# Optimization experiments

Hardware: AMD Instinct MI355X
Metric: run time of the kernel (lower is better)

Reference implementation:

```python
import jax, jax.numpy as jnp
import numpy as np


def setup_inputs() -> dict:
    key = jax.random.key(0)
    k_x, k_q, k_k, k_v = jax.random.split(key, 4)
    B, S, E, D = 4, 2048, 1024, 1024
    scale = 1.0 / np.sqrt(E)
    return {
        "x": jax.random.normal(k_x, (B, S, E), dtype=jnp.float32),
        # nn.Linear weight matrices, shape [out_dim, in_dim]; y = x @ W.T
        "w_q": jax.random.normal(k_q, (D, E), dtype=jnp.float32) * scale,
        "w_k": jax.random.normal(k_k, (D, E), dtype=jnp.float32) * scale,
        "w_v": jax.random.normal(k_v, (D, E), dtype=jnp.float32) * scale,
    }


def reference(x, w_q, w_k, w_v):
    # x: [B, S, E]; w_*: [D, E] (torch nn.Linear convention)
    B, S, E = x.shape
    q = jnp.einsum("bse,de->bsd", x, w_q)  # [B, S, D]
    k = jnp.einsum("bse,de->bsd", x, w_k)
    v = jnp.einsum("bse,de->bsd", x, w_v)
    D = q.shape[-1]
    # raw scores, then causal mask (strictly upper triangle -> -inf), then
    # scale by 1/sqrt(D) inside softmax exactly as the original does.
    scores = jnp.einsum("bsd,btd->bst", q, k)  # [B, S, S]
    causal = jnp.tril(jnp.ones((S, S), dtype=bool))  # True = keep
    scores = jnp.where(causal[None], scores, -jnp.inf)
    attn = jax.nn.softmax(scores / jnp.sqrt(jnp.asarray(D, x.dtype)), axis=-1)
    # dropout p=0.0 -> identity
    return jnp.einsum("bst,btd->bsd", attn, v)  # [B, S, D]
```

## Files before the change

kernel.cpp:

```cpp
#include <hip/hip_runtime.h>
#include <hip/hip_bf16.h>


typedef unsigned short u16;
typedef __attribute__((ext_vector_type(4))) u16   u16x4;
typedef __attribute__((ext_vector_type(8))) u16   u16x8;
typedef __attribute__((ext_vector_type(8))) short short8;
typedef __attribute__((ext_vector_type(4))) float f32x4;

__device__ inline u16 f2b(float v) {
    __hip_bfloat16 b = __float2bfloat16(v);
    return *reinterpret_cast<u16*>(&b);
}
__device__ inline float b2f(u16 v) {
    unsigned int u = ((unsigned int)v) << 16;
    return *reinterpret_cast<float*>(&u);
}

template <typename T> __device__ inline void store_elem(T* p, float v);
template <> __device__ inline void store_elem<float>(float* p, float v) { *p = v; }
template <> __device__ inline void store_elem<u16>(u16* p, float v)     { *p = f2b(v); }

__device__ inline void gload_lds16(const u16* g, u16* l) {
    __builtin_amdgcn_global_load_lds(
        (const __attribute__((address_space(1))) void*)g,
        (__attribute__((address_space(3))) void*)l, 16, 0, 0);
}

__device__ __forceinline__ short8 dsr128(const u16* p) {
    short8 d;
    asm volatile("ds_read_b128 %0, %1"
        : "=v"(d)
        : "v"((unsigned)(unsigned long long)
              (const __attribute__((address_space(3))) u16*)p));
    return d;
}

__global__ __launch_bounds__(256) void cast_all_kernel(
    const float* __restrict__ x,  const float* __restrict__ wq,
    const float* __restrict__ wk, const float* __restrict__ wv,
    u16* __restrict__ dst) {
    int q = blockIdx.x * 256 + threadIdx.x;
    const float* src;
    int sidx;
    if (q < 2097152) { src = x; sidx = q * 4; }
    else {
        int qq = q - 2097152;
        int w  = qq >> 18;
        sidx   = (qq & 262143) * 4;
        src    = (w == 0) ? wq : (w == 1) ? wk : wv;
    }
    float4 v = *(const float4*)(src + sidx);
    u16x4 o;
    o.x = f2b(v.x); o.y = f2b(v.y); o.z = f2b(v.z); o.w = f2b(v.w);
    *(u16x4*)(dst + q * 4) = o;
}

__device__ __forceinline__ void gemm256_core(
    u16* __restrict__ lds,
    const u16* __restrict__ Ab, int lda,
    const u16* __restrict__ Bb, int ldb,
    u16* __restrict__ Cb, int ldc,
    int m0, int n0)
{
    const int tid  = threadIdx.x;
    const int lane = tid & 63;
    const int wave = tid >> 6;
    const int quad = lane >> 4;
    const int r16  = lane & 15;
    const int wm   = wave >> 2;
    const int wn   = wave & 3;

    int gA[2][2], gB[2][2], lA[2][2], lB[2][2];
    {
        const int cswz = ((lane & 3) * 8) ^ (((lane >> 5) & 1) << 4);
        const int rsub = lane >> 2;
#pragma unroll
        for (int u = 0; u < 2; ++u)
#pragma unroll
            for (int j = 0; j < 2; ++j) {
                int s   = j * 8 + wave;
                int sh  = s >> 1, cg = s & 1;
                int rgA = (sh & 3) + (sh >> 2) * 8 + u * 4;
                int rgB = sh + u * 8;
                int cl  = cg * 32 + cswz;
                gA[u][j] = (m0 + rgA * 16 + rsub) * lda + cl;
                gB[u][j] = (n0 + rgB * 16 + rsub) * ldb + cl;
                lA[u][j] = (rgA * 2 + cg) * 512 + lane * 8;
                lB[u][j] = (rgB * 2 + cg) * 512 + lane * 8;
            }
    }

#define STAGE_A(BUF, U, KK) do { \
        gload_lds16(Ab + gA[U][0] + (KK), lds + (BUF)*32768 + lA[U][0]); \
        gload_lds16(Ab + gA[U][1] + (KK), lds + (BUF)*32768 + lA[U][1]); } while (0)
#define STAGE_B(BUF, U, KK) do { \
        gload_lds16(Bb + gB[U][0] + (KK), lds + (BUF)*32768 + 16384 + lB[U][0]); \
        gload_lds16(Bb + gB[U][1] + (KK), lds + (BUF)*32768 + 16384 + lB[U][1]); } while (0)

    const int cswr = (quad * 8) ^ ((r16 >> 3) << 4);
    const int rdA0 = wm * 16 * 512 + r16 * 32 + cswr;
    const int rdB0 = wn * 8  * 512 + r16 * 32 + cswr;

    f32x4 acc[8][4] = {};

    STAGE_B(0, 0, 0);  STAGE_B(0, 1, 0);  STAGE_A(0, 0, 0);  STAGE_A(0, 1, 0);
    STAGE_B(1, 0, 64); STAGE_B(1, 1, 64); STAGE_A(1, 0, 64); STAGE_A(1, 1, 64);
    asm volatile("s_waitcnt vmcnt(8)" ::: "memory");
    __builtin_amdgcn_s_barrier();

    for (int t = 0; t < 16; ++t) {
        const int  buf = t & 1;
        const int  kk2 = t * 64 + 128;
        const bool pf  = (t < 14);
        const u16* Al  = lds + buf * 32768;
        const u16* Bl  = lds + buf * 32768 + 16384;
        short8 bfr[4][2], a01[2][2], a23[2][2], a45[2][2], a67[2][2];

#pragma unroll
        for (int nf = 0; nf < 4; ++nf)
#pragma unroll
            for (int ks = 0; ks < 2; ++ks)
                bfr[nf][ks] = dsr128(&Bl[rdB0 + (nf * 2 + ks) * 512]);
#pragma unroll
        for (int mf = 0; mf < 2; ++mf)
#pragma unroll
            for (int ks = 0; ks < 2; ++ks)
                a01[mf][ks] = dsr128(&Al[rdA0 + (mf * 2 + ks) * 512]);
        __builtin_amdgcn_s_barrier();
#pragma unroll
        for (int mf = 0; mf < 2; ++mf)
#pragma unroll
            for (int ks = 0; ks < 2; ++ks)
                a23[mf][ks] = dsr128(&Al[rdA0 + ((mf + 2) * 2 + ks) * 512]);
        asm volatile("s_waitcnt lgkmcnt(4)" ::: "memory");
        __builtin_amdgcn_sched_barrier(0);
        __builtin_amdgcn_s_setprio(1);
#pragma unroll
        for (int mf = 0; mf < 2; ++mf)
#pragma unroll
            for (int nf = 0; nf < 4; ++nf)
#pragma unroll
                for (int ks = 0; ks < 2; ++ks)
                    acc[mf][nf] = __builtin_amdgcn_mfma_f32_16x16x32_bf16(
                        a01[mf][ks], bfr[nf][ks], acc[mf][nf], 0, 0, 0);
        __builtin_amdgcn_s_setprio(0);
        __builtin_amdgcn_s_barrier();

        if (pf) STAGE_B(buf, 0, kk2);
        __builtin_amdgcn_s_barrier();
#pragma unroll
        for (int mf = 0; mf < 2; ++mf)
#pragma unroll
            for (int ks = 0; ks < 2; ++ks)
                a45[mf][ks] = dsr128(&Al[rdA0 + ((mf + 4) * 2 + ks) * 512]);
        asm volatile("s_waitcnt lgkmcnt(4)" ::: "memory");
        __builtin_amdgcn_sched_barrier(0);
        __builtin_amdgcn_s_setprio(1);
#pragma unroll
        for (int mf = 0; mf < 2; ++mf)
#pragma unroll
            for (int nf = 0; nf < 4; ++nf)
#pragma unroll
                for (int ks = 0; ks < 2; ++ks)
                    acc[mf + 2][nf] = __builtin_amdgcn_mfma_f32_16x16x32_bf16(
                        a23[mf][ks], bfr[nf][ks], acc[mf + 2][nf], 0, 0, 0);
        __builtin_amdgcn_s_setprio(0);
        __builtin_amdgcn_s_barrier();

        if (pf) { STAGE_B(buf, 1, kk2); STAGE_A(buf, 0, kk2); }
        __builtin_amdgcn_s_barrier();
#pragma unroll
        for (int mf = 0; mf < 2; ++mf)
#pragma unroll
            for (int ks = 0; ks < 2; ++ks)
                a67[mf][ks] = dsr128(&Al[rdA0 + ((mf + 6) * 2 + ks) * 512]);
        asm volatile("s_waitcnt lgkmcnt(4)" ::: "memory");
        __builtin_amdgcn_sched_barrier(0);
        __builtin_amdgcn_s_setprio(1);
#pragma unroll
        for (int mf = 0; mf < 2; ++mf)
#pragma unroll
            for (int nf = 0; nf < 4; ++nf)
#pragma unroll
                for (int ks = 0; ks < 2; ++ks)
                    acc[mf + 4][nf] = __builtin_amdgcn_mfma_f32_16x16x32_bf16(
                        a45[mf][ks], bfr[nf][ks], acc[mf + 4][nf], 0, 0, 0);
        __builtin_amdgcn_s_setprio(0);
        __builtin_amdgcn_s_barrier();

        __builtin_amdgcn_s_barrier();
        asm volatile("s_waitcnt lgkmcnt(0)" ::: "memory");
        __builtin_amdgcn_sched_barrier(0);
        __builtin_amdgcn_s_setprio(1);
#pragma unroll
        for (int mf = 0; mf < 2; ++mf)
#pragma unroll
            for (int nf = 0; nf < 4; ++nf)
#pragma unroll
                for (int ks = 0; ks < 2; ++ks)
                    acc[mf + 6][nf] = __builtin_amdgcn_mfma_f32_16x16x32_bf16(
                        a67[mf][ks], bfr[nf][ks], acc[mf + 6][nf], 0, 0, 0);
        __builtin_amdgcn_s_setprio(0);
        if (pf) STAGE_A(buf, 1, kk2);
        if (pf) asm volatile("s_waitcnt vmcnt(8)" ::: "memory");
        else    asm volatile("s_waitcnt vmcnt(0)" ::: "memory");
        __builtin_amdgcn_s_barrier();
    }
#undef STAGE_A
#undef STAGE_B

#pragma unroll
    for (int mf = 0; mf < 8; ++mf) {
        int m = m0 + wm * 128 + mf * 16 + quad * 4;
#pragma unroll
        for (int nf = 0; nf < 4; ++nf) {
            int n = n0 + wn * 64 + nf * 16 + r16;
#pragma unroll
            for (int r = 0; r < 4; ++r)
                Cb[(m + r) * ldc + n] = f2b(acc[mf][nf][r]);
        }
    }
}

__global__ __launch_bounds__(512) void gemm_qk256(
    const u16* __restrict__ xb, const u16* __restrict__ wb,
    u16* __restrict__ qk)
{
    __shared__ __align__(16) u16 lds[2 * 2 * 16384];
    int flat = blockIdx.x;
    int swz  = (flat & 7) * 32 + (flat >> 3);
    int m0   = (swz >> 3) * 256;
    int n0   = (swz & 7) * 256;
    gemm256_core(lds, xb, 1024, wb, 1024, qk, 2048, m0, n0);
}

__global__ __launch_bounds__(512) void gemm_sc256(
    const u16* __restrict__ qk, u16* __restrict__ sc)
{
    __shared__ __align__(16) u16 lds[2 * 2 * 16384];
    int flat = blockIdx.x;
    int swz  = (flat & 7) * 18 + (flat >> 3);
    int z    = swz / 36;
    int t    = swz - z * 36;
    float ff = sqrtf(8.0f * t + 1.0f);
    int m = (int)((ff - 1.0f) * 0.5f);
    while ((m + 1) * (m + 2) / 2 <= t) m++;
    while (m * (m + 1) / 2 > t) m--;
    int n = t - m * (m + 1) / 2;
    const u16* Ab = qk + (long long)z * 2048 * 2048;
    gemm256_core(lds, Ab, 2048, Ab + 1024, 2048,
                 sc + (long long)z * 2048 * 2048, 2048, m * 256, n * 256);
}

#define MT 128
#define NT 128
#define BKH 32
#define HSZ (MT * BKH)

template <int TRANS, typename OutT>
__device__ __forceinline__ void gemm_core(
    u16* __restrict__ As, u16* __restrict__ Bs,
    const u16* __restrict__ Ab, int lda,
    const u16* __restrict__ Bb, int ldb,
    OutT* __restrict__ Cb, int ldc,
    int m0, int n0, int kbeg, int kend)
{
    const int tid  = threadIdx.x;
    const int lane = tid & 63;
    const int wave = tid >> 6;
    const int quad = lane >> 4;
    const int r16  = lane & 15;
    const int mw   = (wave >> 1) * 64;
    const int nw   = (wave & 1) * 64;

    const int c0 = tid, c1 = tid + 256;
    const int r0 = c0 >> 2, k0 = (c0 & 3) * 8;
    const int r1 = c1 >> 2, k1 = (c1 & 3) * 8;
    const int oa0 = (m0 + r0) * lda + k0;
    const int oa1 = (m0 + r1) * lda + k1;
    const int ob0 = (n0 + r0) * ldb + k0;
    const int ob1 = (n0 + r1) * ldb + k1;

    f32x4 acc[4][4] = {};

    for (int kk = kbeg; kk < kend; kk += 2 * BKH) {
        __syncthreads();
        gload_lds16(Ab + (kk + oa0),        &As[c0 * 8]);
        gload_lds16(Ab + (kk + oa1),        &As[c1 * 8]);
        gload_lds16(Ab + (kk + BKH + oa0),  &As[HSZ + c0 * 8]);
        gload_lds16(Ab + (kk + BKH + oa1),  &As[HSZ + c1 * 8]);
        gload_lds16(Bb + (kk + ob0),        &Bs[c0 * 8]);
        gload_lds16(Bb + (kk + ob1),        &Bs[c1 * 8]);
        gload_lds16(Bb + (kk + BKH + ob0),  &Bs[HSZ + c0 * 8]);
        gload_lds16(Bb + (kk + BKH + ob1),  &Bs[HSZ + c1 * 8]);
        __syncthreads();

#pragma unroll
        for (int h = 0; h < 2; h++) {
            short8 af[4], bf[4];
#pragma unroll
            for (int i = 0; i < 4; i++)
                af[i] = *(const short8*)&As[h * HSZ + (mw + i * 16 + r16) * BKH + quad * 8];
#pragma unroll
            for (int j = 0; j < 4; j++)
                bf[j] = *(const short8*)&Bs[h * HSZ + (nw + j * 16 + r16) * BKH + quad * 8];
#pragma unroll
            for (int i = 0; i < 4; i++)
#pragma unroll
                for (int j = 0; j < 4; j++)
                    acc[i][j] = __builtin_amdgcn_mfma_f32_16x16x32_bf16(af[i], bf[j], acc[i][j], 0, 0, 0);
        }
    }

    if (TRANS == 0) {
#pragma unroll
        for (int i = 0; i < 4; i++)
#pragma unroll
            for (int j = 0; j < 4; j++)
#pragma unroll
                for (int r = 0; r < 4; r++) {
                    int m = m0 + mw + i * 16 + quad * 4 + r;
                    int n = n0 + nw + j * 16 + r16;
                    store_elem(&Cb[(long long)m * ldc + n], acc[i][j][r]);
                }
    } else {
#pragma unroll
        for (int i = 0; i < 4; i++)
#pragma unroll
            for (int j = 0; j < 4; j++) {
                int mbase = m0 + mw + i * 16 + quad * 4;
                int d     = n0 + nw + j * 16 + r16;
                int b     = mbase >> 11;
                int s     = mbase & 2047;
                u16x4 o;
#pragma unroll
                for (int r = 0; r < 4; r++) o[r] = f2b(acc[i][j][r]);
                *(u16x4*)((u16*)Cb + (((b << 10) + d) * 2048 + s)) = o;
            }
    }
}

__device__ __forceinline__ void softmax_row(const u16* __restrict__ sc,
                                            u16* __restrict__ P, int row,
                                            float* __restrict__ red) {
    const int S = 2048;
    int i   = row & (S - 1);
    int n   = i + 1;
    int kendr = (i & ~127) + 128;
    const u16* srow = sc + (long long)row * S;
    u16*       prow = P  + (long long)row * S;

    int j0 = threadIdx.x * 8;
    u16x8 raw = {};
    if (j0 <= i) raw = *(const u16x8*)(srow + j0);
    float v[8];
#pragma unroll
    for (int e = 0; e < 8; e++) v[e] = (j0 + e < n) ? b2f(raw[e]) : -1e30f;

    float lmax = v[0];
#pragma unroll
    for (int e = 1; e < 8; e++) lmax = fmaxf(lmax, v[e]);
    for (int o = 32; o > 0; o >>= 1) lmax = fmaxf(lmax, __shfl_xor(lmax, o, 64));
    int wid = threadIdx.x >> 6;
    if ((threadIdx.x & 63) == 0) red[wid] = lmax;
    __syncthreads();
    float Mx = fmaxf(fmaxf(red[0], red[1]), fmaxf(red[2], red[3]));

    const float C = 0.045112384f;
    float ev[8];
    float lsum = 0.f;
#pragma unroll
    for (int e = 0; e < 8; e++) {
        ev[e] = (j0 + e < n) ? exp2f((v[e] - Mx) * C) : 0.f;
        lsum += ev[e];
    }
    for (int o = 32; o > 0; o >>= 1) lsum += __shfl_xor(lsum, o, 64);
    if ((threadIdx.x & 63) == 0) red[4 + wid] = lsum;
    __syncthreads();
    float inv = 1.0f / (red[4] + red[5] + red[6] + red[7]);

    if (j0 < kendr) {
        u16x8 o8;
#pragma unroll
        for (int e = 0; e < 8; e++) o8[e] = f2b(ev[e] * inv);
        *(u16x8*)(prow + j0) = o8;
    }
}

__global__ __launch_bounds__(256, 4) void v_softmax(
    const u16* __restrict__ xb, const u16* __restrict__ wb,
    u16* __restrict__ vt,
    const u16* __restrict__ sc, u16* __restrict__ P)
{
    __shared__ __align__(16) u16 As[2 * HSZ];
    __shared__ __align__(16) u16 Bs[2 * HSZ];
    int bid = blockIdx.x;
    if (bid < 512) {
        int vb = (bid & 7) * 64 + (bid >> 3);
        int m0 = (vb >> 3) * MT;
        int n0 = (vb & 7) * NT;
        gemm_core<1, u16>(As, Bs, xb, 1024, wb + 2048 * 1024, 1024, vt, 2048,
                          m0, n0, 0, 1024);
    } else {
        float* red = (float*)As;
        int sid = bid - 512;
        int z = sid >> 10, i = sid & 1023;
        softmax_row(sc, P, z * 2048 + (2047 - i), red);
        softmax_row(sc, P, z * 2048 + i, red);
    }
}

__global__ __launch_bounds__(256, 4) void gemm_pv(
    const u16* __restrict__ P, const u16* __restrict__ vt,
    float* __restrict__ out)
{
    __shared__ __align__(16) u16 As[2 * HSZ];
    __shared__ __align__(16) u16 Bs[2 * HSZ];
    const int bid = blockIdx.x;
    const int m  = (bid < 256) ? (15 - (bid >> 5)) : ((bid - 256) >> 5);
    const int nz = bid & 31;
    const int n  = nz & 7;
    const int z  = nz >> 3;
    const int m0 = m * MT;

    gemm_core<0, float>(As, Bs,
        P  + (long long)z * 2048 * 2048, 2048,
        vt + (long long)z * 1024 * 2048, 2048,
        out + (long long)z * 2097152, 1024,
        m0, n * NT, 0, m0 + MT);
}

extern "C" void kernel_launch(void* const* d_in, const int* in_sizes, int n_in,
                              void* d_out, int out_size, void* d_ws, size_t ws_size,
                              hipStream_t stream) {
    const float* x  = (const float*)d_in[0];
    const float* wq = (const float*)d_in[1];
    const float* wk = (const float*)d_in[2];
    const float* wv = (const float*)d_in[3];
    float* out = (float*)d_out;

    char* ws = (char*)d_ws;
    u16*   xb   = (u16*)(ws);
    u16*   wb   = (u16*)(ws + 16777216LL);
    u16*   qk   = (u16*)(ws + 23068672LL);
    u16*   sc   = (u16*)(ws + 56623104LL);
    u16*   P    = (u16*)(ws + 90177536LL);
    u16*   vt   = (u16*)(ws + 123731968LL);

    cast_all_kernel<<<11264, 256, 0, stream>>>(x, wq, wk, wv, xb);

    gemm_qk256<<<256, 512, 0, stream>>>(xb, wb, qk);

    gemm_sc256<<<144, 512, 0, stream>>>(qk, sc);

    v_softmax<<<4608, 256, 0, stream>>>(xb, wb, vt, sc, P);

    gemm_pv<<<512, 256, 0, stream>>>(P, vt, out);
}
```

Baseline: 229.2 us.

## Fuse five launches into two cooperative kernels with grid-wide syncs

Merges the cast, QK projection and score GEMM into one cooperative kernel separated by grid.sync, and merges the V projection, causal softmax and PV GEMM into a second cooperative kernel. The aim is to remove launch gaps and tail idle time between the five separate kernels. In exchange, the launches are persistent grids: 256 blocks do the cast in a loop, and the softmax rows are spread over 512 blocks. Grid barriers also leave most blocks idle during the score GEMM, and occupancy is lower than with the earlier 4608-block softmax launch.

```diff
diff --git a/kernel.cpp b/kernel.cpp
--- a/kernel.cpp
+++ b/kernel.cpp
@@ -1,6 +1,9 @@
 #include <hip/hip_runtime.h>
 #include <hip/hip_bf16.h>
-
+#include <hip/hip_cooperative_groups.h>
+
+
+namespace cg = cooperative_groups;
 
 typedef unsigned short u16;
 typedef __attribute__((ext_vector_type(4))) u16   u16x4;
@@ -34,26 +37,6 @@
         : "v"((unsigned)(unsigned long long)
               (const __attribute__((address_space(3))) u16*)p));
     return d;
-}
-
-__global__ __launch_bounds__(256) void cast_all_kernel(
-    const float* __restrict__ x,  const float* __restrict__ wq,
-    const float* __restrict__ wk, const float* __restrict__ wv,
-    u16* __restrict__ dst) {
-    int q = blockIdx.x * 256 + threadIdx.x;
-    const float* src;
-    int sidx;
-    if (q < 2097152) { src = x; sidx = q * 4; }
-    else {
-        int qq = q - 2097152;
-        int w  = qq >> 18;
-        sidx   = (qq & 262143) * 4;
-        src    = (w == 0) ? wq : (w == 1) ? wk : wv;
-    }
-    float4 v = *(const float4*)(src + sidx);
-    u16x4 o;
-    o.x = f2b(v.x); o.y = f2b(v.y); o.z = f2b(v.z); o.w = f2b(v.w);
-    *(u16x4*)(dst + q * 4) = o;
 }
 
 __device__ __forceinline__ void gemm256_core(
@@ -80,14 +63,14 @@
 #pragma unroll
             for (int j = 0; j < 2; ++j) {
                 int s   = j * 8 + wave;
-                int sh  = s >> 1, cg = s & 1;
+                int sh  = s >> 1, cg2 = s & 1;
                 int rgA = (sh & 3) + (sh >> 2) * 8 + u * 4;
                 int rgB = sh + u * 8;
-                int cl  = cg * 32 + cswz;
+                int cl  = cg2 * 32 + cswz;
                 gA[u][j] = (m0 + rgA * 16 + rsub) * lda + cl;
                 gB[u][j] = (n0 + rgB * 16 + rsub) * ldb + cl;
-                lA[u][j] = (rgA * 2 + cg) * 512 + lane * 8;
-                lB[u][j] = (rgB * 2 + cg) * 512 + lane * 8;
+                lA[u][j] = (rgA * 2 + cg2) * 512 + lane * 8;
+                lB[u][j] = (rgB * 2 + cg2) * 512 + lane * 8;
             }
     }
 
@@ -221,36 +204,6 @@
                 Cb[(m + r) * ldc + n] = f2b(acc[mf][nf][r]);
         }
     }
-}
-
-__global__ __launch_bounds__(512) void gemm_qk256(
-    const u16* __restrict__ xb, const u16* __restrict__ wb,
-    u16* __restrict__ qk)
-{
-    __shared__ __align__(16) u16 lds[2 * 2 * 16384];
-    int flat = blockIdx.x;
-    int swz  = (flat & 7) * 32 + (flat >> 3);
-    int m0   = (swz >> 3) * 256;
-    int n0   = (swz & 7) * 256;
-    gemm256_core(lds, xb, 1024, wb, 1024, qk, 2048, m0, n0);
-}
-
-__global__ __launch_bounds__(512) void gemm_sc256(
-    const u16* __restrict__ qk, u16* __restrict__ sc)
-{
-    __shared__ __align__(16) u16 lds[2 * 2 * 16384];
-    int flat = blockIdx.x;
-    int swz  = (flat & 7) * 18 + (flat >> 3);
-    int z    = swz / 36;
-    int t    = swz - z * 36;
-    float ff = sqrtf(8.0f * t + 1.0f);
-    int m = (int)((ff - 1.0f) * 0.5f);
-    while ((m + 1) * (m + 2) / 2 <= t) m++;
-    while (m * (m + 1) / 2 > t) m--;
-    int n = t - m * (m + 1) / 2;
-    const u16* Ab = qk + (long long)z * 2048 * 2048;
-    gemm256_core(lds, Ab, 2048, Ab + 1024, 2048,
-                 sc + (long long)z * 2048 * 2048, 2048, m * 256, n * 256);
 }
 
 #define MT 128
@@ -386,49 +339,107 @@
         for (int e = 0; e < 8; e++) o8[e] = f2b(ev[e] * inv);
         *(u16x8*)(prow + j0) = o8;
     }
-}
-
-__global__ __launch_bounds__(256, 4) void v_softmax(
+    __syncthreads();
+}
+
+__global__ __launch_bounds__(512) void front_fused(
+    const float* __restrict__ x,  const float* __restrict__ wq,
+    const float* __restrict__ wk, const float* __restrict__ wv,
+    u16* __restrict__ xb, const u16* __restrict__ wb,
+    u16* __restrict__ qk, u16* __restrict__ sc)
+{
+    __shared__ __align__(16) u16 lds[2 * 2 * 16384];
+    cg::grid_group grid = cg::this_grid();
+    const int tid  = threadIdx.x;
+    const int flat = blockIdx.x;
+
+#pragma unroll 2
+    for (int k = 0; k < 22; ++k) {
+        int q = k * 131072 + flat * 512 + tid;
+        const float* src; int sidx;
+        if (q < 2097152) { src = x; sidx = q * 4; }
+        else {
+            int qq = q - 2097152;
+            int w  = qq >> 18;
+            sidx   = (qq & 262143) * 4;
+            src    = (w == 0) ? wq : (w == 1) ? wk : wv;
+        }
+        float4 v = *(const float4*)(src + sidx);
+        u16x4 o;
+        o.x = f2b(v.x); o.y = f2b(v.y); o.z = f2b(v.z); o.w = f2b(v.w);
+        *(u16x4*)(xb + q * 4) = o;
+    }
+    __threadfence();
+    grid.sync();
+
+    {
+        int swz = (flat & 7) * 32 + (flat >> 3);
+        int m0  = (swz >> 3) * 256;
+        int n0  = (swz & 7) * 256;
+        gemm256_core(lds, xb, 1024, wb, 1024, qk, 2048, m0, n0);
+    }
+    __threadfence();
+    grid.sync();
+
+    if (flat < 144) {
+        int swz = (flat & 7) * 18 + (flat >> 3);
+        int z   = swz / 36;
+        int t   = swz - z * 36;
+        float ff = sqrtf(8.0f * t + 1.0f);
+        int m = (int)((ff - 1.0f) * 0.5f);
+        while ((m + 1) * (m + 2) / 2 <= t) m++;
+        while (m * (m + 1) / 2 > t) m--;
+        int n = t - m * (m + 1) / 2;
+        const u16* Ab = qk + (long long)z * 2048 * 2048;
+        gemm256_core(lds, Ab, 2048, Ab + 1024, 2048,
+                     sc + (long long)z * 2048 * 2048, 2048, m * 256, n * 256);
+    }
+}
+
+__global__ __launch_bounds__(256, 2) void back_fused(
     const u16* __restrict__ xb, const u16* __restrict__ wb,
-    u16* __restrict__ vt,
-    const u16* __restrict__ sc, u16* __restrict__ P)
+    u16* __restrict__ vt, const u16* __restrict__ sc,
+    u16* __restrict__ P, float* __restrict__ out)
 {
     __shared__ __align__(16) u16 As[2 * HSZ];
     __shared__ __align__(16) u16 Bs[2 * HSZ];
-    int bid = blockIdx.x;
-    if (bid < 512) {
+    cg::grid_group grid = cg::this_grid();
+    const int bid = blockIdx.x;
+
+    {
         int vb = (bid & 7) * 64 + (bid >> 3);
         int m0 = (vb >> 3) * MT;
         int n0 = (vb & 7) * NT;
         gemm_core<1, u16>(As, Bs, xb, 1024, wb + 2048 * 1024, 1024, vt, 2048,
                           m0, n0, 0, 1024);
-    } else {
+    }
+    __syncthreads();
+
+    {
         float* red = (float*)As;
-        int sid = bid - 512;
-        int z = sid >> 10, i = sid & 1023;
-        softmax_row(sc, P, z * 2048 + (2047 - i), red);
-        softmax_row(sc, P, z * 2048 + i, red);
-    }
-}
-
-__global__ __launch_bounds__(256, 4) void gemm_pv(
-    const u16* __restrict__ P, const u16* __restrict__ vt,
-    float* __restrict__ out)
-{
-    __shared__ __align__(16) u16 As[2 * HSZ];
-    __shared__ __align__(16) u16 Bs[2 * HSZ];
-    const int bid = blockIdx.x;
-    const int m  = (bid < 256) ? (15 - (bid >> 5)) : ((bid - 256) >> 5);
-    const int nz = bid & 31;
-    const int n  = nz & 7;
-    const int z  = nz >> 3;
-    const int m0 = m * MT;
-
-    gemm_core<0, float>(As, Bs,
-        P  + (long long)z * 2048 * 2048, 2048,
-        vt + (long long)z * 1024 * 2048, 2048,
-        out + (long long)z * 2097152, 1024,
-        m0, n * NT, 0, m0 + MT);
+        int p0 = bid * 8;
+#pragma unroll 1
+        for (int p = p0; p < p0 + 8; ++p) {
+            int z = p >> 10, i = p & 1023;
+            softmax_row(sc, P, z * 2048 + (2047 - i), red);
+            softmax_row(sc, P, z * 2048 + i, red);
+        }
+    }
+    __threadfence();
+    grid.sync();
+
+    {
+        const int m  = (bid < 256) ? (15 - (bid >> 5)) : ((bid - 256) >> 5);
+        const int nz = bid & 31;
+        const int n  = nz & 7;
+        const int z  = nz >> 3;
+        const int m0 = m * MT;
+        gemm_core<0, float>(As, Bs,
+            P  + (long long)z * 2048 * 2048, 2048,
+            vt + (long long)z * 1024 * 2048, 2048,
+            out + (long long)z * 2097152, 1024,
+            m0, n * NT, 0, m0 + MT);
+    }
 }
 
 extern "C" void kernel_launch(void* const* d_in, const int* in_sizes, int n_in,
@@ -441,20 +452,23 @@
     float* out = (float*)d_out;
 
     char* ws = (char*)d_ws;
-    u16*   xb   = (u16*)(ws);
-    u16*   wb   = (u16*)(ws + 16777216LL);
-    u16*   qk   = (u16*)(ws + 23068672LL);
-    u16*   sc   = (u16*)(ws + 56623104LL);
-    u16*   P    = (u16*)(ws + 90177536LL);
-    u16*   vt   = (u16*)(ws + 123731968LL);
-
-    cast_all_kernel<<<11264, 256, 0, stream>>>(x, wq, wk, wv, xb);
-
-    gemm_qk256<<<256, 512, 0, stream>>>(xb, wb, qk);
-
-    gemm_sc256<<<144, 512, 0, stream>>>(qk, sc);
-
-    v_softmax<<<4608, 256, 0, stream>>>(xb, wb, vt, sc, P);
-
-    gemm_pv<<<512, 256, 0, stream>>>(P, vt, out);
-}
+    u16* xb = (u16*)(ws);
+    u16* wb = (u16*)(ws + 16777216LL);
+    u16* qk = (u16*)(ws + 23068672LL);
+    u16* sc = (u16*)(ws + 56623104LL);
+    u16* P  = (u16*)(ws + 90177536LL);
+    u16* vt = (u16*)(ws + 123731968LL);
+
+    {
+        void* args[] = {(void*)&x, (void*)&wq, (void*)&wk, (void*)&wv,
+                        (void*)&xb, (void*)&wb, (void*)&qk, (void*)&sc};
+        hipLaunchCooperativeKernel((const void*)front_fused,
+                                   dim3(256), dim3(512), args, 0, stream);
+    }
+    {
+        void* args[] = {(void*)&xb, (void*)&wb, (void*)&vt, (void*)&sc,
+                        (void*)&P, (void*)&out};
+        hipLaunchCooperativeKernel((const void*)back_fused,
+                                   dim3(512), dim3(256), args, 0, stream);
+    }
+}
```

After: 540.5 us. 2.36x slower.

## Co-schedule V projection with causal score GEMM, split softmax into own kernel

Applied to the files above, without the earlier changes.

The V projection moves out of the softmax kernel and into the same launch as the causal QK^T score GEMM, filling 64 extra 512-thread blocks beside the 144 score tiles. Each extra block runs two independent 256-thread halves, and each half loops over four 128x128 output tiles. Softmax becomes a standalone launch. The aim is to fill CUs left idle by the triangular 144-block score GEMM. The cost is that the V-projection work is now packed into fewer, longer blocks, which may become the critical path of that launch.

```diff
diff --git a/kernel.cpp b/kernel.cpp
--- a/kernel.cpp
+++ b/kernel.cpp
@@ -80,14 +80,14 @@
 #pragma unroll
             for (int j = 0; j < 2; ++j) {
                 int s   = j * 8 + wave;
-                int sh  = s >> 1, cg = s & 1;
+                int sh  = s >> 1, cg2 = s & 1;
                 int rgA = (sh & 3) + (sh >> 2) * 8 + u * 4;
                 int rgB = sh + u * 8;
-                int cl  = cg * 32 + cswz;
+                int cl  = cg2 * 32 + cswz;
                 gA[u][j] = (m0 + rgA * 16 + rsub) * lda + cl;
                 gB[u][j] = (n0 + rgB * 16 + rsub) * ldb + cl;
-                lA[u][j] = (rgA * 2 + cg) * 512 + lane * 8;
-                lB[u][j] = (rgB * 2 + cg) * 512 + lane * 8;
+                lA[u][j] = (rgA * 2 + cg2) * 512 + lane * 8;
+                lB[u][j] = (rgB * 2 + cg2) * 512 + lane * 8;
             }
     }
 
@@ -235,24 +235,6 @@
     gemm256_core(lds, xb, 1024, wb, 1024, qk, 2048, m0, n0);
 }
 
-__global__ __launch_bounds__(512) void gemm_sc256(
-    const u16* __restrict__ qk, u16* __restrict__ sc)
-{
-    __shared__ __align__(16) u16 lds[2 * 2 * 16384];
-    int flat = blockIdx.x;
-    int swz  = (flat & 7) * 18 + (flat >> 3);
-    int z    = swz / 36;
-    int t    = swz - z * 36;
-    float ff = sqrtf(8.0f * t + 1.0f);
-    int m = (int)((ff - 1.0f) * 0.5f);
-    while ((m + 1) * (m + 2) / 2 <= t) m++;
-    while (m * (m + 1) / 2 > t) m--;
-    int n = t - m * (m + 1) / 2;
-    const u16* Ab = qk + (long long)z * 2048 * 2048;
-    gemm256_core(lds, Ab, 2048, Ab + 1024, 2048,
-                 sc + (long long)z * 2048 * 2048, 2048, m * 256, n * 256);
-}
-
 #define MT 128
 #define NT 128
 #define BKH 32
@@ -260,13 +242,13 @@
 
 template <int TRANS, typename OutT>
 __device__ __forceinline__ void gemm_core(
+    const int tid,
     u16* __restrict__ As, u16* __restrict__ Bs,
     const u16* __restrict__ Ab, int lda,
     const u16* __restrict__ Bb, int ldb,
     OutT* __restrict__ Cb, int ldc,
     int m0, int n0, int kbeg, int kend)
 {
-    const int tid  = threadIdx.x;
     const int lane = tid & 63;
     const int wave = tid >> 6;
     const int quad = lane >> 4;
@@ -341,6 +323,42 @@
     }
 }
 
+__global__ __launch_bounds__(512) void gemm_scv(
+    const u16* __restrict__ qk, u16* __restrict__ sc,
+    const u16* __restrict__ xb, const u16* __restrict__ wb,
+    u16* __restrict__ vt)
+{
+    __shared__ __align__(16) u16 lds[2 * 2 * 16384];
+    int flat = blockIdx.x;
+    if (flat < 144) {
+        int swz = (flat & 7) * 18 + (flat >> 3);
+        int z   = swz / 36;
+        int t   = swz - z * 36;
+        float ff = sqrtf(8.0f * t + 1.0f);
+        int m = (int)((ff - 1.0f) * 0.5f);
+        while ((m + 1) * (m + 2) / 2 <= t) m++;
+        while (m * (m + 1) / 2 > t) m--;
+        int n = t - m * (m + 1) / 2;
+        const u16* Ab = qk + (long long)z * 2048 * 2048;
+        gemm256_core(lds, Ab, 2048, Ab + 1024, 2048,
+                     sc + (long long)z * 2048 * 2048, 2048, m * 256, n * 256);
+    } else {
+        int b  = flat - 144;
+        int vb = (b & 7) * 8 + (b >> 3);
+        int m0 = vb * MT;
+        int h   = threadIdx.x >> 8;
+        int tid = threadIdx.x & 255;
+        u16* As = lds + h * 16384;
+        u16* Bs = lds + h * 16384 + 8192;
+#pragma unroll 1
+        for (int s = 0; s < 4; ++s) {
+            int n0 = (s * 2 + h) * NT;
+            gemm_core<1, u16>(tid, As, Bs, xb, 1024, wb + 2048 * 1024, 1024,
+                              vt, 2048, m0, n0, 0, 1024);
+        }
+    }
+}
+
 __device__ __forceinline__ void softmax_row(const u16* __restrict__ sc,
                                             u16* __restrict__ P, int row,
                                             float* __restrict__ red) {
@@ -388,27 +406,13 @@
     }
 }
 
-__global__ __launch_bounds__(256, 4) void v_softmax(
-    const u16* __restrict__ xb, const u16* __restrict__ wb,
-    u16* __restrict__ vt,
-    const u16* __restrict__ sc, u16* __restrict__ P)
-{
-    __shared__ __align__(16) u16 As[2 * HSZ];
-    __shared__ __align__(16) u16 Bs[2 * HSZ];
-    int bid = blockIdx.x;
-    if (bid < 512) {
-        int vb = (bid & 7) * 64 + (bid >> 3);
-        int m0 = (vb >> 3) * MT;
-        int n0 = (vb & 7) * NT;
-        gemm_core<1, u16>(As, Bs, xb, 1024, wb + 2048 * 1024, 1024, vt, 2048,
-                          m0, n0, 0, 1024);
-    } else {
-        float* red = (float*)As;
-        int sid = bid - 512;
-        int z = sid >> 10, i = sid & 1023;
-        softmax_row(sc, P, z * 2048 + (2047 - i), red);
-        softmax_row(sc, P, z * 2048 + i, red);
-    }
+__global__ __launch_bounds__(256) void softmax_kernel(const u16* __restrict__ sc,
+                                                      u16* __restrict__ P) {
+    __shared__ float red[8];
+    int i = blockIdx.x;
+    int z = blockIdx.z;
+    softmax_row(sc, P, z * 2048 + (2047 - i), red);
+    softmax_row(sc, P, z * 2048 + i, red);
 }
 
 __global__ __launch_bounds__(256, 4) void gemm_pv(
@@ -424,7 +428,7 @@
     const int z  = nz >> 3;
     const int m0 = m * MT;
 
-    gemm_core<0, float>(As, Bs,
+    gemm_core<0, float>(threadIdx.x, As, Bs,
         P  + (long long)z * 2048 * 2048, 2048,
         vt + (long long)z * 1024 * 2048, 2048,
         out + (long long)z * 2097152, 1024,
@@ -441,20 +445,20 @@
     float* out = (float*)d_out;
 
     char* ws = (char*)d_ws;
-    u16*   xb   = (u16*)(ws);
-    u16*   wb   = (u16*)(ws + 16777216LL);
-    u16*   qk   = (u16*)(ws + 23068672LL);
-    u16*   sc   = (u16*)(ws + 56623104LL);
-    u16*   P    = (u16*)(ws + 90177536LL);
-    u16*   vt   = (u16*)(ws + 123731968LL);
+    u16* xb = (u16*)(ws);
+    u16* wb = (u16*)(ws + 16777216LL);
+    u16* qk = (u16*)(ws + 23068672LL);
+    u16* sc = (u16*)(ws + 56623104LL);
+    u16* P  = (u16*)(ws + 90177536LL);
+    u16* vt = (u16*)(ws + 123731968LL);
 
     cast_all_kernel<<<11264, 256, 0, stream>>>(x, wq, wk, wv, xb);
 
     gemm_qk256<<<256, 512, 0, stream>>>(xb, wb, qk);
 
-    gemm_sc256<<<144, 512, 0, stream>>>(qk, sc);
-
-    v_softmax<<<4608, 256, 0, stream>>>(xb, wb, vt, sc, P);
+    gemm_scv<<<208, 512, 0, stream>>>(qk, sc, xb, wb, vt);
+
+    softmax_kernel<<<dim3(1024, 1, 4), 256, 0, stream>>>(sc, P);
 
     gemm_pv<<<512, 256, 0, stream>>>(P, vt, out);
 }
```

Measured after the change: 294.1 us. +28.3%, slower.
